# Kernel tuning notes

Measured on AMD Instinct MI355X. Metric: run time of the kernel, lower is better.

Reference implementation:

```python
import jax, jax.numpy as jnp
import numpy as np

C = 18          # channels (hardcoded in repo)
K = 7           # depthwise kernel size
R = 16          # CBAM reduction -> bottleneck = C // R = 1
B, L = 16, 131072
EPS = 1e-6


def setup_inputs() -> dict:
    key = jax.random.key(0)
    ks = jax.random.split(key, 10)
    Cb = C // R  # 1
    return {
        "x":     jax.random.normal(ks[0], (B, C, L), dtype=jnp.float32),
        "dw_w":  jax.random.normal(ks[1], (C, 1, K), dtype=jnp.float32) * 0.1,   # depthwise Conv1d weight (O, I/g, K)
        "dw_b":  jax.random.normal(ks[2], (C,), dtype=jnp.float32) * 0.1,
        "ln_w":  jnp.ones((C,), dtype=jnp.float32),
        "ln_b":  jnp.zeros((C,), dtype=jnp.float32),
        "w1":    jax.random.normal(ks[3], (4 * C, C), dtype=jnp.float32) * 0.1,  # Linear: (out, in)
        "b1":    jax.random.normal(ks[4], (4 * C,), dtype=jnp.float32) * 0.1,
        "w2":    jax.random.normal(ks[5], (C, 4 * C), dtype=jnp.float32) * 0.1,
        "b2":    jax.random.normal(ks[6], (C,), dtype=jnp.float32) * 0.1,
        "gamma": jnp.full((C,), 1e-6, dtype=jnp.float32),                        # layer scale
        "ca_w1": jax.random.normal(ks[7], (Cb, C), dtype=jnp.float32) * 0.1,     # 1x1 Conv1d, no bias
        "ca_w2": jax.random.normal(ks[8], (C, Cb), dtype=jnp.float32) * 0.1,
    }


def reference(x, dw_w, dw_b, ln_w, ln_b, w1, b1, w2, b2, gamma, ca_w1, ca_w2):
    residual = x                                   # (B, C, L)
    pad = K // 2
    y = jax.lax.conv_general_dilated(
        x, dw_w, window_strides=(1,), padding=[(pad, pad)],
        dimension_numbers=("NCH", "OIH", "NCH"), feature_group_count=C,
    ) + dw_b[None, :, None]                        # depthwise conv, 'same'

    y = y.transpose(0, 2, 1)                       # (B, L, C) channels_last
    mu = y.mean(-1, keepdims=True)
    var = ((y - mu) ** 2).mean(-1, keepdims=True)  # biased var, as F.layer_norm
    y = (y - mu) / jnp.sqrt(var + EPS) * ln_w + ln_b

    y = jax.nn.gelu(y @ w1.T + b1, approximate=False)   # (B, L, 4C), exact GELU
    y = y @ w2.T + b2                                   # (B, L, C)
    y = gamma * y                                       # layer scale
    y = y.transpose(0, 2, 1)                            # (B, C, L)

    # ChannelAttention (CBAM channel branch): shared MLP on avg- and max-pooled descriptors
    avg = y.mean(-1)                               # (B, C)
    mx = y.max(-1)                                 # (B, C)
    def fc(v):
        return jax.nn.relu(v @ ca_w1.T) @ ca_w2.T  # (B, C)
    att = jax.nn.sigmoid(fc(avg) + fc(mx))         # (B, C)
    y = y * att[:, :, None]

    return jax.nn.gelu(y + residual, approximate=False)
```

## Files before the change

### kernel.cpp

```cpp
#include <hip/hip_runtime.h>
#include <hip/hip_bf16.h>
#include <math.h>

#define CCH   18
#define KW    7
#define LLEN  131072
#define BATCH 16
#define EPSV  1e-6f
#define HID   72

#define BLOCK 256
#define POSB  256
#define TILES 4
#define POS_PER_BLK (POSB * TILES)
#define BPBLK (LLEN / POS_PER_BLK)

typedef __attribute__((ext_vector_type(8))) short short8;
typedef __attribute__((ext_vector_type(4))) float f32x4;
typedef __attribute__((ext_vector_type(4))) unsigned uint4v;

#define OFF_W2S  5120
#define SMEM_SZ  20480

__device__ __forceinline__ float gelu_exact(float v) {
    return 0.5f * v * (1.0f + erff(v * 0.70710678118654752f));
}
__device__ __forceinline__ float gelu_fast(float u) {
    float s = fmaf(0.25f, u, 0.5f);
    s = __builtin_fminf(__builtin_fmaxf(s, 0.0f), 1.0f);
    return u * s;
}
__device__ __forceinline__ unsigned short to_bf(float f) {
    return __builtin_bit_cast(unsigned short, __float2bfloat16(f));
}
__device__ __forceinline__ float bf2f(unsigned short u) {
    return __uint_as_float((unsigned)u << 16);
}
__device__ __forceinline__ unsigned pk2(float lo, float hi) {
    return (unsigned)to_bf(lo) | ((unsigned)to_bf(hi) << 16);
}

__device__ __forceinline__ void ystore(float* p, float v) { *p = v; }
__device__ __forceinline__ void ystore(__hip_bfloat16* p, float v) { *p = __float2bfloat16(v); }

template<typename YT>
__global__ __launch_bounds__(BLOCK, 4) void k1_main(
    const float* __restrict__ x,
    const float* __restrict__ dw_w, const float* __restrict__ dw_b,
    const float* __restrict__ ln_w, const float* __restrict__ ln_b,
    const float* __restrict__ w1,   const float* __restrict__ b1,
    const float* __restrict__ w2,   const float* __restrict__ b2,
    const float* __restrict__ gamma,
    YT* __restrict__ y_out,
    float* __restrict__ psum, float* __restrict__ pmax)
{
    __shared__ __align__(16) char smem[SMEM_SZ];
    float*          xsf  = (float*)smem;
    unsigned short* w1l  = (unsigned short*)smem;
    unsigned short* w2l  = (unsigned short*)(smem + OFF_W2S);

    const int tid  = threadIdx.x;
    const int b    = blockIdx.x / BPBLK;
    const int blk  = blockIdx.x % BPBLK;
    const int xbase = b * CCH * LLEN;
    const int base_l = blk * POS_PER_BLK;
    const int lane = tid & 63, w = tid >> 6;
    const int g = lane >> 4, c16 = lane & 15;

    const float beta = 1.143f;
    const float hu = bf2f(to_bf(gelu_fast(bf2f(to_bf(beta)))));

    for (int i = tid; i < 80 * 32; i += BLOCK) {
        const int h = i >> 5, c = i & 31;
        float val = 0.0f;
        if (h < HID) {
            if (c < CCH) val = w1[h * CCH + c];
            else if (c == CCH) val = b1[h];
        } else if (h == HID && c == CCH) val = beta;
        w1l[i] = to_bf(val);
    }
    for (int i = tid; i < CCH * 96; i += BLOCK) {
        const int c = i / 96, h = i % 96;
        float val = 0.0f;
        if (h < HID) val = w2[c * HID + h] * gamma[c];
        else if (h == HID) val = b2[c] * gamma[c] / hu;
        w2l[i] = to_bf(val);
    }
    if (tid < 92) ((uint4*)(smem + 19008))[tid] = make_uint4(0, 0, 0, 0);
    __syncthreads();

    short8 a1[5];
    #pragma unroll
    for (int mt = 0; mt < 5; ++mt)
        a1[mt] = *(const short8*)(w1l + (mt * 16 + c16) * 32 + g * 8);
    short8 a2[2][3];
    const short8 z8 = (short8)0;
    #pragma unroll
    for (int ks = 0; ks < 3; ++ks) {
        a2[0][ks] = *(const short8*)(w2l + c16 * 96 + ks * 32 + g * 8);
        const int r2 = 16 + c16;
        const int rc = (r2 < CCH) ? r2 : 0;
        const short8 t = *(const short8*)(w2l + rc * 96 + ks * 32 + g * 8);
        a2[1][ks] = (r2 < CCH) ? t : z8;
    }

    const int addrA = (((lane >> 4) & 1) * 32 + c16) << 2;
    const int addrB = addrA + 64;
    const bool selB = (lane & 32) != 0;

    float ysum0[4] = {0.f, 0.f, 0.f, 0.f};
    float ymax0[4] = {-INFINITY, -INFINITY, -INFINITY, -INFINITY};
    float ysum1[2] = {0.f, 0.f};
    float ymax1[2] = {-INFINITY, -INFINITY};

    for (int t = 0; t < TILES; ++t) {
        const int lt0 = base_l + t * POSB;
        const int q0 = lt0 / 4;
        __syncthreads();

        for (int i = tid; i < CCH * 66; i += BLOCK) {
            const int c = i / 66, qi = i % 66;
            const int q = q0 - 1 + qi;
            float4 vv = make_float4(0.f, 0.f, 0.f, 0.f);
            if (q >= 0 && q < LLEN / 4)
                vv = *((const float4*)(x + xbase + c * LLEN) + q);
            ((float4*)smem)[i] = vv;
        }
        __syncthreads();

        float v[CCH];
        #pragma unroll
        for (int c = 0; c < CCH; ++c) {
            const float* row = xsf + c * 264;
            float acc = dw_b[c];
            #pragma unroll
            for (int k = 0; k < KW; ++k)
                acc = fmaf(row[tid + 1 + k], dw_w[c * KW + k], acc);
            v[c] = acc;
        }
        {
            float mu = 0.0f;
            #pragma unroll
            for (int c = 0; c < CCH; ++c) mu += v[c];
            mu *= (1.0f / CCH);
            float var = 0.0f;
            #pragma unroll
            for (int c = 0; c < CCH; ++c) { const float d = v[c] - mu; var = fmaf(d, d, var); }
            var *= (1.0f / CCH);
            const float rs = __builtin_amdgcn_rsqf(var + EPSV);
            #pragma unroll
            for (int c = 0; c < CCH; ++c)
                v[c] = (v[c] - mu) * rs * ln_w[c] + ln_b[c];
        }
        __syncthreads();

        {
            unsigned pk[16];
            #pragma unroll
            for (int cc = 0; cc < 9; ++cc) pk[cc] = pk2(v[2 * cc], v[2 * cc + 1]);
            pk[9] = 0x3F80u;
            #pragma unroll
            for (int cc = 10; cc < 16; ++cc) pk[cc] = 0u;
            uint4* dst = (uint4*)(smem + tid * 80);
            dst[0] = make_uint4(pk[0], pk[1], pk[2], pk[3]);
            dst[1] = make_uint4(pk[4], pk[5], pk[6], pk[7]);
            dst[2] = make_uint4(pk[8], pk[9], pk[10], pk[11]);
            dst[3] = make_uint4(pk[12], pk[13], pk[14], pk[15]);
        }

        #pragma unroll
        for (int nt = 0; nt < 4; ++nt) {
            const short8 bf = *(const short8*)(smem + (w * 64 + nt * 16 + c16) * 80 + g * 16);

            f32x4 acc1[5];
            #pragma unroll
            for (int mt = 0; mt < 5; ++mt) {
                f32x4 z = {0.f, 0.f, 0.f, 0.f};
                acc1[mt] = __builtin_amdgcn_mfma_f32_16x16x32_bf16(a1[mt], bf, z, 0, 0, 0);
            }

            int pkh[5][2];
            #pragma unroll
            for (int mt = 0; mt < 5; ++mt) {
                const float h0 = gelu_fast(acc1[mt][0]);
                const float h1 = gelu_fast(acc1[mt][1]);
                const float h2 = gelu_fast(acc1[mt][2]);
                const float h3 = gelu_fast(acc1[mt][3]);
                pkh[mt][0] = (int)pk2(h0, h1);
                pkh[mt][1] = (int)pk2(h2, h3);
            }

            f32x4 acc2_0 = {0.f, 0.f, 0.f, 0.f};
            f32x4 acc2_1 = {0.f, 0.f, 0.f, 0.f};
            #pragma unroll
            for (int ks = 0; ks < 2; ++ks) {
                const int l0x = __builtin_amdgcn_ds_bpermute(addrA, pkh[2 * ks][0]);
                const int l0y = __builtin_amdgcn_ds_bpermute(addrA, pkh[2 * ks][1]);
                const int l1x = __builtin_amdgcn_ds_bpermute(addrA, pkh[2 * ks + 1][0]);
                const int l1y = __builtin_amdgcn_ds_bpermute(addrA, pkh[2 * ks + 1][1]);
                const int h0x = __builtin_amdgcn_ds_bpermute(addrB, pkh[2 * ks][0]);
                const int h0y = __builtin_amdgcn_ds_bpermute(addrB, pkh[2 * ks][1]);
                const int h1x = __builtin_amdgcn_ds_bpermute(addrB, pkh[2 * ks + 1][0]);
                const int h1y = __builtin_amdgcn_ds_bpermute(addrB, pkh[2 * ks + 1][1]);
                uint4v hu4;
                hu4.x = (unsigned)(selB ? l1x : l0x);
                hu4.y = (unsigned)(selB ? l1y : l0y);
                hu4.z = (unsigned)(selB ? h1x : h0x);
                hu4.w = (unsigned)(selB ? h1y : h0y);
                const short8 hb = __builtin_bit_cast(short8, hu4);
                acc2_0 = __builtin_amdgcn_mfma_f32_16x16x32_bf16(a2[0][ks], hb, acc2_0, 0, 0, 0);
                acc2_1 = __builtin_amdgcn_mfma_f32_16x16x32_bf16(a2[1][ks], hb, acc2_1, 0, 0, 0);
            }
            {
                const int lx = __builtin_amdgcn_ds_bpermute(addrA, pkh[4][0]);
                const int ly = __builtin_amdgcn_ds_bpermute(addrA, pkh[4][1]);
                const int hx = __builtin_amdgcn_ds_bpermute(addrB, pkh[4][0]);
                const int hy = __builtin_amdgcn_ds_bpermute(addrB, pkh[4][1]);
                uint4v hu4;
                hu4.x = selB ? 0u : (unsigned)lx;
                hu4.y = selB ? 0u : (unsigned)ly;
                hu4.z = selB ? 0u : (unsigned)hx;
                hu4.w = selB ? 0u : (unsigned)hy;
                const short8 hb = __builtin_bit_cast(short8, hu4);
                acc2_0 = __builtin_amdgcn_mfma_f32_16x16x32_bf16(a2[0][2], hb, acc2_0, 0, 0, 0);
                acc2_1 = __builtin_amdgcn_mfma_f32_16x16x32_bf16(a2[1][2], hb, acc2_1, 0, 0, 0);
            }

            YT* yb = y_out + xbase + lt0 + w * 64 + nt * 16 + c16;
            #pragma unroll
            for (int r = 0; r < 4; ++r) {
                ystore(yb + (4 * g + r) * LLEN, acc2_0[r]);
                ysum0[r] += acc2_0[r];
                ymax0[r] = fmaxf(ymax0[r], acc2_0[r]);
            }
            if (g == 0) {
                ystore(yb + 16 * LLEN, acc2_1[0]);
                ystore(yb + 17 * LLEN, acc2_1[1]);
                ysum1[0] += acc2_1[0];  ymax1[0] = fmaxf(ymax1[0], acc2_1[0]);
                ysum1[1] += acc2_1[1];  ymax1[1] = fmaxf(ymax1[1], acc2_1[1]);
            }
        }
    }

    __syncthreads();
    float* redS = (float*)smem;
    float* redM = (float*)smem + 72;
    #pragma unroll
    for (int off = 1; off < 16; off <<= 1) {
        #pragma unroll
        for (int r = 0; r < 4; ++r) {
            ysum0[r] += __shfl_xor(ysum0[r], off, 64);
            ymax0[r] = fmaxf(ymax0[r], __shfl_xor(ymax0[r], off, 64));
        }
        #pragma unroll
        for (int r = 0; r < 2; ++r) {
            ysum1[r] += __shfl_xor(ysum1[r], off, 64);
            ymax1[r] = fmaxf(ymax1[r], __shfl_xor(ymax1[r], off, 64));
        }
    }
    if (c16 == 0) {
        #pragma unroll
        for (int r = 0; r < 4; ++r) {
            redS[w * CCH + 4 * g + r] = ysum0[r];
            redM[w * CCH + 4 * g + r] = ymax0[r];
        }
        if (g == 0) {
            redS[w * CCH + 16] = ysum1[0];  redM[w * CCH + 16] = ymax1[0];
            redS[w * CCH + 17] = ysum1[1];  redM[w * CCH + 17] = ymax1[1];
        }
    }
    __syncthreads();
    if (tid < CCH) {
        const float s = redS[tid] + redS[CCH + tid] + redS[2 * CCH + tid] + redS[3 * CCH + tid];
        const float m = fmaxf(fmaxf(redM[tid], redM[CCH + tid]),
                              fmaxf(redM[2 * CCH + tid], redM[3 * CCH + tid]));
        psum[blockIdx.x * CCH + tid] = s;
        pmax[blockIdx.x * CCH + tid] = m;
    }
}

__global__ __launch_bounds__(64) void k2_att(
    const float* __restrict__ psum, const float* __restrict__ pmax,
    const float* __restrict__ ca_w1, const float* __restrict__ ca_w2,
    float* __restrict__ att)
{
    const int b = blockIdx.x;
    const int c = threadIdx.x;
    __shared__ float av[CCH], mx[CCH], gate;
    if (c < CCH) {
        float s = 0.0f, m = -INFINITY;
        for (int k = 0; k < BPBLK; ++k) {
            s += psum[(b * BPBLK + k) * CCH + c];
            m = fmaxf(m, pmax[(b * BPBLK + k) * CCH + c]);
        }
        av[c] = s * (1.0f / LLEN);
        mx[c] = m;
    }
    __syncthreads();
    if (c == 0) {
        float a = 0.0f, m = 0.0f;
        #pragma unroll
        for (int i = 0; i < CCH; ++i) {
            a = fmaf(av[i], ca_w1[i], a);
            m = fmaf(mx[i], ca_w1[i], m);
        }
        gate = fmaxf(a, 0.0f) + fmaxf(m, 0.0f);
    }
    __syncthreads();
    if (c < CCH) {
        const float t = gate * ca_w2[c];
        att[b * CCH + c] = 1.0f / (1.0f + expf(-t));
    }
}

template<typename YT>
__global__ __launch_bounds__(256) void k3_final(
    const float* __restrict__ x, const float* __restrict__ att,
    const YT* __restrict__ y, float* __restrict__ out)
{
    const int i4 = blockIdx.x * 256 + threadIdx.x;
    const int row = (i4 * 4) >> 17;
    const float a = att[row];

    float yv[4];
    if constexpr (sizeof(YT) == 2) {
        const ushort4 t = ((const ushort4*)y)[i4];
        yv[0] = bf2f(t.x); yv[1] = bf2f(t.y); yv[2] = bf2f(t.z); yv[3] = bf2f(t.w);
    } else {
        const float4 t = ((const float4*)y)[i4];
        yv[0] = t.x; yv[1] = t.y; yv[2] = t.z; yv[3] = t.w;
    }
    const float4 xv = ((const float4*)x)[i4];
    float4 r;
    r.x = gelu_exact(fmaf(a, yv[0], xv.x));
    r.y = gelu_exact(fmaf(a, yv[1], xv.y));
    r.z = gelu_exact(fmaf(a, yv[2], xv.z));
    r.w = gelu_exact(fmaf(a, yv[3], xv.w));
    ((float4*)out)[i4] = r;
}

extern "C" void kernel_launch(void* const* d_in, const int* in_sizes, int n_in,
                              void* d_out, int out_size, void* d_ws, size_t ws_size,
                              hipStream_t stream) {
    const float* x     = (const float*)d_in[0];
    const float* dw_w  = (const float*)d_in[1];
    const float* dw_b  = (const float*)d_in[2];
    const float* ln_w  = (const float*)d_in[3];
    const float* ln_b  = (const float*)d_in[4];
    const float* w1    = (const float*)d_in[5];
    const float* b1    = (const float*)d_in[6];
    const float* w2    = (const float*)d_in[7];
    const float* b2    = (const float*)d_in[8];
    const float* gamma = (const float*)d_in[9];
    const float* ca_w1 = (const float*)d_in[10];
    const float* ca_w2 = (const float*)d_in[11];

    float* out = (float*)d_out;
    const size_t nelem  = (size_t)BATCH * CCH * LLEN;
    const size_t ybytes = nelem * 2;
    const size_t pbytes = (size_t)BATCH * BPBLK * CCH * 4;
    const int total4 = (int)(nelem / 4);

    if (ws_size >= ybytes + 2 * pbytes + 4096) {
        __hip_bfloat16* y = (__hip_bfloat16*)d_ws;
        float* psum = (float*)((char*)d_ws + ybytes);
        float* pmax = psum + (size_t)BATCH * BPBLK * CCH;
        float* att  = pmax + (size_t)BATCH * BPBLK * CCH;

        k1_main<__hip_bfloat16><<<BATCH * BPBLK, BLOCK, 0, stream>>>(
            x, dw_w, dw_b, ln_w, ln_b, w1, b1, w2, b2, gamma, y, psum, pmax);
        k2_att<<<BATCH, 64, 0, stream>>>(psum, pmax, ca_w1, ca_w2, att);
        k3_final<__hip_bfloat16><<<total4 / 256, 256, 0, stream>>>(x, att, y, out);
    } else {
        float* ws   = (float*)d_ws;
        float* psum = ws;
        float* pmax = psum + (size_t)BATCH * BPBLK * CCH;
        float* att  = pmax + (size_t)BATCH * BPBLK * CCH;

        k1_main<float><<<BATCH * BPBLK, BLOCK, 0, stream>>>(
            x, dw_w, dw_b, ln_w, ln_b, w1, b1, w2, b2, gamma, out, psum, pmax);
        k2_att<<<BATCH, 64, 0, stream>>>(psum, pmax, ca_w1, ca_w2, att);
        k3_final<float><<<total4 / 256, 256, 0, stream>>>(x, att, out, out);
    }
}
```

Measured before the change: 190.2 us.

## Permute W2 columns to consume MFMA outputs directly, drop ds_bpermute shuffles

Reorders the hidden dimension of the second-layer weight matrix in shared memory so the packed GELU outputs of the first MFMA can feed the second MFMA as the B operand directly. This removes the 20 ds_bpermute cross-lane shuffles and selects per 16-position tile. Weights now live in a separate padded LDS region and are reloaded from LDS at each MFMA instead of being held in registers, which frees VGPRs but adds LDS reads and grows shared memory from 20 KB to about 30 KB.

```diff
diff --git a/kernel.cpp b/kernel.cpp
--- a/kernel.cpp
+++ b/kernel.cpp
@@ -19,8 +19,9 @@
 typedef __attribute__((ext_vector_type(4))) float f32x4;
 typedef __attribute__((ext_vector_type(4))) unsigned uint4v;
 
-#define OFF_W2S  5120
-#define SMEM_SZ  20480
+#define OFF_W1L  20480
+#define OFF_W2L  26880
+#define SMEM_SZ  30624
 
 __device__ __forceinline__ float gelu_exact(float v) {
     return 0.5f * v * (1.0f + erff(v * 0.70710678118654752f));
@@ -42,6 +43,16 @@
 
 __device__ __forceinline__ void ystore(float* p, float v) { *p = v; }
 __device__ __forceinline__ void ystore(__hip_bfloat16* p, float v) { *p = __float2bfloat16(v); }
+
+__device__ __forceinline__ int w2perm(int k) {
+    const int ks32 = k & ~31;
+    const int rem  = k & 31;
+    const int g    = rem >> 3;
+    const int t    = rem & 7;
+    const int j    = t >> 1;
+    const int eps  = t & 1;
+    return ks32 + ((j & 2) << 3) + (g << 2) + ((j & 1) << 1) + eps;
+}
 
 template<typename YT>
 __global__ __launch_bounds__(BLOCK, 4) void k1_main(
@@ -55,9 +66,9 @@
     float* __restrict__ psum, float* __restrict__ pmax)
 {
     __shared__ __align__(16) char smem[SMEM_SZ];
-    float*          xsf  = (float*)smem;
-    unsigned short* w1l  = (unsigned short*)smem;
-    unsigned short* w2l  = (unsigned short*)(smem + OFF_W2S);
+    float*          xsf = (float*)smem;
+    unsigned short* w1l = (unsigned short*)(smem + OFF_W1L);
+    unsigned short* w2x = (unsigned short*)(smem + OFF_W2L);
 
     const int tid  = threadIdx.x;
     const int b    = blockIdx.x / BPBLK;
@@ -70,8 +81,8 @@
     const float beta = 1.143f;
     const float hu = bf2f(to_bf(gelu_fast(bf2f(to_bf(beta)))));
 
-    for (int i = tid; i < 80 * 32; i += BLOCK) {
-        const int h = i >> 5, c = i & 31;
+    for (int i = tid; i < 80 * 40; i += BLOCK) {
+        const int h = i / 40, c = i % 40;
         float val = 0.0f;
         if (h < HID) {
             if (c < CCH) val = w1[h * CCH + c];
@@ -79,34 +90,22 @@
         } else if (h == HID && c == CCH) val = beta;
         w1l[i] = to_bf(val);
     }
-    for (int i = tid; i < CCH * 96; i += BLOCK) {
-        const int c = i / 96, h = i % 96;
+    for (int i = tid; i < CCH * 104; i += BLOCK) {
+        const int c = i / 104, k = i % 104;
         float val = 0.0f;
-        if (h < HID) val = w2[c * HID + h] * gamma[c];
-        else if (h == HID) val = b2[c] * gamma[c] / hu;
-        w2l[i] = to_bf(val);
-    }
-    if (tid < 92) ((uint4*)(smem + 19008))[tid] = make_uint4(0, 0, 0, 0);
-    __syncthreads();
-
-    short8 a1[5];
-    #pragma unroll
-    for (int mt = 0; mt < 5; ++mt)
-        a1[mt] = *(const short8*)(w1l + (mt * 16 + c16) * 32 + g * 8);
-    short8 a2[2][3];
-    const short8 z8 = (short8)0;
-    #pragma unroll
-    for (int ks = 0; ks < 3; ++ks) {
-        a2[0][ks] = *(const short8*)(w2l + c16 * 96 + ks * 32 + g * 8);
-        const int r2 = 16 + c16;
-        const int rc = (r2 < CCH) ? r2 : 0;
-        const short8 t = *(const short8*)(w2l + rc * 96 + ks * 32 + g * 8);
-        a2[1][ks] = (r2 < CCH) ? t : z8;
-    }
-
-    const int addrA = (((lane >> 4) & 1) * 32 + c16) << 2;
-    const int addrB = addrA + 64;
-    const bool selB = (lane & 32) != 0;
+        if (k < 96) {
+            const int h = w2perm(k);
+            if (h < HID)       val = w2[c * HID + h] * gamma[c];
+            else if (h == HID) val = b2[c] * gamma[c] / hu;
+        }
+        w2x[i] = to_bf(val);
+    }
+    __syncthreads();
+
+    const int a1base = c16 * 40 + g * 8;
+    const int a2base0 = c16 * 104 + g * 8;
+    const int rcB = (c16 < 2) ? (16 + c16) : 17;
+    const int a2base1 = rcB * 104 + g * 8;
 
     float ysum0[4] = {0.f, 0.f, 0.f, 0.f};
     float ymax0[4] = {-INFINITY, -INFINITY, -INFINITY, -INFINITY};
@@ -176,54 +175,35 @@
             #pragma unroll
             for (int mt = 0; mt < 5; ++mt) {
                 f32x4 z = {0.f, 0.f, 0.f, 0.f};
-                acc1[mt] = __builtin_amdgcn_mfma_f32_16x16x32_bf16(a1[mt], bf, z, 0, 0, 0);
-            }
-
-            int pkh[5][2];
+                const short8 a1f = *(const short8*)(w1l + mt * 640 + a1base);
+                acc1[mt] = __builtin_amdgcn_mfma_f32_16x16x32_bf16(a1f, bf, z, 0, 0, 0);
+            }
+
+            unsigned pkh[5][2];
             #pragma unroll
             for (int mt = 0; mt < 5; ++mt) {
                 const float h0 = gelu_fast(acc1[mt][0]);
                 const float h1 = gelu_fast(acc1[mt][1]);
                 const float h2 = gelu_fast(acc1[mt][2]);
                 const float h3 = gelu_fast(acc1[mt][3]);
-                pkh[mt][0] = (int)pk2(h0, h1);
-                pkh[mt][1] = (int)pk2(h2, h3);
+                pkh[mt][0] = pk2(h0, h1);
+                pkh[mt][1] = pk2(h2, h3);
             }
 
             f32x4 acc2_0 = {0.f, 0.f, 0.f, 0.f};
             f32x4 acc2_1 = {0.f, 0.f, 0.f, 0.f};
             #pragma unroll
-            for (int ks = 0; ks < 2; ++ks) {
-                const int l0x = __builtin_amdgcn_ds_bpermute(addrA, pkh[2 * ks][0]);
-                const int l0y = __builtin_amdgcn_ds_bpermute(addrA, pkh[2 * ks][1]);
-                const int l1x = __builtin_amdgcn_ds_bpermute(addrA, pkh[2 * ks + 1][0]);
-                const int l1y = __builtin_amdgcn_ds_bpermute(addrA, pkh[2 * ks + 1][1]);
-                const int h0x = __builtin_amdgcn_ds_bpermute(addrB, pkh[2 * ks][0]);
-                const int h0y = __builtin_amdgcn_ds_bpermute(addrB, pkh[2 * ks][1]);
-                const int h1x = __builtin_amdgcn_ds_bpermute(addrB, pkh[2 * ks + 1][0]);
-                const int h1y = __builtin_amdgcn_ds_bpermute(addrB, pkh[2 * ks + 1][1]);
+            for (int ks = 0; ks < 3; ++ks) {
                 uint4v hu4;
-                hu4.x = (unsigned)(selB ? l1x : l0x);
-                hu4.y = (unsigned)(selB ? l1y : l0y);
-                hu4.z = (unsigned)(selB ? h1x : h0x);
-                hu4.w = (unsigned)(selB ? h1y : h0y);
+                hu4.x = pkh[2 * ks][0];
+                hu4.y = pkh[2 * ks][1];
+                hu4.z = (ks < 2) ? pkh[2 * ks + 1][0] : pkh[4][0];
+                hu4.w = (ks < 2) ? pkh[2 * ks + 1][1] : pkh[4][1];
                 const short8 hb = __builtin_bit_cast(short8, hu4);
-                acc2_0 = __builtin_amdgcn_mfma_f32_16x16x32_bf16(a2[0][ks], hb, acc2_0, 0, 0, 0);
-                acc2_1 = __builtin_amdgcn_mfma_f32_16x16x32_bf16(a2[1][ks], hb, acc2_1, 0, 0, 0);
-            }
-            {
-                const int lx = __builtin_amdgcn_ds_bpermute(addrA, pkh[4][0]);
-                const int ly = __builtin_amdgcn_ds_bpermute(addrA, pkh[4][1]);
-                const int hx = __builtin_amdgcn_ds_bpermute(addrB, pkh[4][0]);
-                const int hy = __builtin_amdgcn_ds_bpermute(addrB, pkh[4][1]);
-                uint4v hu4;
-                hu4.x = selB ? 0u : (unsigned)lx;
-                hu4.y = selB ? 0u : (unsigned)ly;
-                hu4.z = selB ? 0u : (unsigned)hx;
-                hu4.w = selB ? 0u : (unsigned)hy;
-                const short8 hb = __builtin_bit_cast(short8, hu4);
-                acc2_0 = __builtin_amdgcn_mfma_f32_16x16x32_bf16(a2[0][2], hb, acc2_0, 0, 0, 0);
-                acc2_1 = __builtin_amdgcn_mfma_f32_16x16x32_bf16(a2[1][2], hb, acc2_1, 0, 0, 0);
+                const short8 a20 = *(const short8*)(w2x + a2base0 + ks * 32);
+                const short8 a21 = *(const short8*)(w2x + a2base1 + ks * 32);
+                acc2_0 = __builtin_amdgcn_mfma_f32_16x16x32_bf16(a20, hb, acc2_0, 0, 0, 0);
+                acc2_1 = __builtin_amdgcn_mfma_f32_16x16x32_bf16(a21, hb, acc2_1, 0, 0, 0);
             }
 
             YT* yb = y_out + xbase + lt0 + w * 64 + nt * 16 + c16;
```

New measurement: 183.1 us. 1.04x faster.
